# Kernel tuning notes

Hardware: AMD Instinct MI355X
Metric: run time of the kernel (lower is better)

Reference implementation:

```python
import jax, jax.numpy as jnp
import numpy as np

S, D_IN, D_OUT = 4096, 1024, 1024

def setup_inputs() -> dict:
    key = jax.random.key(0)
    kx, kq, kk, kv = jax.random.split(key, 4)
    scale = 0.02
    return {
        "x": jax.random.normal(kx, (S, D_IN), dtype=jnp.float32),
        "W_query": jax.random.normal(kq, (D_IN, D_OUT), dtype=jnp.float32) * scale,
        "W_key": jax.random.normal(kk, (D_IN, D_OUT), dtype=jnp.float32) * scale,
        "W_value": jax.random.normal(kv, (D_IN, D_OUT), dtype=jnp.float32) * scale,
    }

def reference(x, W_query, W_key, W_value):
    # x: [S, d_in]; W_*: [d_in, d_out]
    queries = x @ W_query        # [S, d_out]
    keys = x @ W_key             # [S, d_out]
    values = x @ W_value         # [S, d_out]
    d_k = keys.shape[-1]
    attn_scores = queries @ keys.T            # [S, S]
    attn_weights = jax.nn.softmax(attn_scores / jnp.sqrt(jnp.float32(d_k)), axis=-1)
    context_vec = attn_weights @ values       # [S, d_out]
    return context_vec
```

## Files before the change

### kernel.cpp

```cpp
#include <hip/hip_runtime.h>

typedef _Float16 f16x8 __attribute__((ext_vector_type(8)));
typedef float f32x4 __attribute__((ext_vector_type(4)));
typedef unsigned short u16;
typedef u16 u16x8 __attribute__((ext_vector_type(8)));
typedef u16 u16x4 __attribute__((ext_vector_type(4)));

__device__ __forceinline__ u16 f2h_bits(float f) {
    _Float16 h = (_Float16)f;
    return __builtin_bit_cast(u16, h);
}
__device__ __forceinline__ float h2f(u16 b) {
    return (float)__builtin_bit_cast(_Float16, b);
}

typedef __attribute__((address_space(1))) unsigned int gu32_as1;
typedef __attribute__((address_space(3))) unsigned int lu32_as3;
__device__ __forceinline__ void gload16(const u16* g, u16* l) {
    __builtin_amdgcn_global_load_lds((gu32_as1*)g, (lu32_as3*)l, 16, 0, 0);
}

template <int MODE>
__global__ __launch_bounds__(512, 2) void gemm_bt(
    const u16* __restrict__ A, int lda,
    const u16* __restrict__ B, int ldb,
    u16* __restrict__ C, int ldc,
    int Ksplit, float alpha, size_t c_z_stride,
    int bnW, int bmW, int numPanelX,
    float* __restrict__ rowsum, u16* __restrict__ vt)
{
    __shared__ __attribute__((aligned(16))) u16 As[32768];
    __shared__ __attribute__((aligned(16))) u16 Bs[32768];

    const int t    = threadIdx.x;
    const int lane = t & 63;
    const int wave = t >> 6;
    const int wm   = wave >> 2;
    const int wn   = wave & 3;
    const int l16  = lane & 15;
    const int quad = lane >> 4;

    const int lin = blockIdx.y * gridDim.x + blockIdx.x;
    const int xcd = lin & 7;
    const int idx = lin >> 3;
    const int px  = xcd % numPanelX;
    const int py  = xcd / numPanelX;
    const int bn  = px * bnW + idx % bnW;
    const int bm  = py * bmW + idx / bnW;

    const int kz = blockIdx.z;
    A += (size_t)kz * Ksplit;
    B += (size_t)kz * Ksplit;
    C += (size_t)kz * c_z_stride;

    const int srow = t >> 2;
    const int sseg = (t & 3) ^ ((t >> 3) & 3);

    const u16* gA = A + (size_t)(bm * 256 + srow) * lda + sseg * 8;
    const u16* gB = B + (size_t)(bn * 256 + srow) * ldb + sseg * 8;
    const size_t a128 = (size_t)128 * lda;
    const size_t b128 = (size_t)128 * ldb;

    u16* lA = As + t * 8;
    u16* lB = Bs + t * 8;

#define STAGE_A(bufv, kt) do {                                   \
        const u16* _g = gA + (size_t)(kt) * 64;                  \
        u16* _l = lA + (bufv) * 16384;                           \
        gload16(_g,             _l);                             \
        gload16(_g + 32,        _l + 4096);                      \
        gload16(_g + a128,      _l + 8192);                      \
        gload16(_g + a128 + 32, _l + 12288);                     \
    } while (0)
#define STAGE_B(bufv, kt) do {                                   \
        const u16* _g = gB + (size_t)(kt) * 64;                  \
        u16* _l = lB + (bufv) * 16384;                           \
        gload16(_g,             _l);                             \
        gload16(_g + 32,        _l + 4096);                      \
        gload16(_g + b128,      _l + 8192);                      \
        gload16(_g + b128 + 32, _l + 12288);                     \
    } while (0)

    const int fslot = quad ^ ((l16 >> 1) & 3);
    const u16* Afr = As + wm * 8192 + l16 * 32 + fslot * 8;
    const u16* Bfr = Bs + (wn >> 1) * 8192 + (wn & 1) * 2048 + l16 * 32 + fslot * 8;

    f32x4 acc[8][4] = {};

    const int NT = Ksplit >> 6;

    STAGE_A(0, 0); STAGE_B(0, 0);
    STAGE_A(1, 1); STAGE_B(1, 1);
    asm volatile("s_waitcnt vmcnt(8)" ::: "memory");
    __builtin_amdgcn_sched_barrier(0);
    __builtin_amdgcn_s_barrier();

    int buf = 0;
    for (int kt = 0; kt < NT; ++kt, buf ^= 1) {
        const u16* Af = Afr + buf * 16384;
        const u16* Bf = Bfr + buf * 16384;
        f16x8 af[4][2], bfA[2][2], bfB[2][2];

#pragma unroll
        for (int mi = 0; mi < 4; mi++)
#pragma unroll
            for (int kk = 0; kk < 2; kk++)
                af[mi][kk] = *(const f16x8*)(Af + kk * 4096 + mi * 512);
#pragma unroll
        for (int nj = 0; nj < 2; nj++)
#pragma unroll
            for (int kk = 0; kk < 2; kk++)
                bfA[nj][kk] = *(const f16x8*)(Bf + kk * 4096 + nj * 512);
        __builtin_amdgcn_sched_barrier(0);
        __builtin_amdgcn_s_barrier();
        __builtin_amdgcn_s_setprio(1);
#pragma unroll
        for (int mi = 0; mi < 4; mi++)
#pragma unroll
            for (int nj = 0; nj < 2; nj++)
#pragma unroll
                for (int kk = 0; kk < 2; kk++)
                    acc[mi][nj] = __builtin_amdgcn_mfma_f32_16x16x32_f16(
                        af[mi][kk], bfA[nj][kk], acc[mi][nj], 0, 0, 0);
        __builtin_amdgcn_s_setprio(0);
        __builtin_amdgcn_sched_barrier(0);
        __builtin_amdgcn_s_barrier();

#pragma unroll
        for (int nj = 0; nj < 2; nj++)
#pragma unroll
            for (int kk = 0; kk < 2; kk++)
                bfB[nj][kk] = *(const f16x8*)(Bf + kk * 4096 + (2 + nj) * 512);
        __builtin_amdgcn_sched_barrier(0);
        __builtin_amdgcn_s_barrier();
        __builtin_amdgcn_s_setprio(1);
#pragma unroll
        for (int mi = 0; mi < 4; mi++)
#pragma unroll
            for (int nj = 0; nj < 2; nj++)
#pragma unroll
                for (int kk = 0; kk < 2; kk++)
                    acc[mi][2 + nj] = __builtin_amdgcn_mfma_f32_16x16x32_f16(
                        af[mi][kk], bfB[nj][kk], acc[mi][2 + nj], 0, 0, 0);
        __builtin_amdgcn_s_setprio(0);
        __builtin_amdgcn_sched_barrier(0);
        __builtin_amdgcn_s_barrier();

#pragma unroll
        for (int mi = 0; mi < 4; mi++)
#pragma unroll
            for (int kk = 0; kk < 2; kk++)
                af[mi][kk] = *(const f16x8*)(Af + kk * 4096 + (4 + mi) * 512);
        if (kt + 2 < NT) STAGE_B(buf, kt + 2);
        __builtin_amdgcn_sched_barrier(0);
        __builtin_amdgcn_s_barrier();
        __builtin_amdgcn_s_setprio(1);
#pragma unroll
        for (int mi = 0; mi < 4; mi++)
#pragma unroll
            for (int nj = 0; nj < 2; nj++)
#pragma unroll
                for (int kk = 0; kk < 2; kk++)
                    acc[4 + mi][nj] = __builtin_amdgcn_mfma_f32_16x16x32_f16(
                        af[mi][kk], bfA[nj][kk], acc[4 + mi][nj], 0, 0, 0);
        __builtin_amdgcn_s_setprio(0);
        __builtin_amdgcn_sched_barrier(0);
        __builtin_amdgcn_s_barrier();

        if (kt + 2 < NT) STAGE_A(buf, kt + 2);
        __builtin_amdgcn_sched_barrier(0);
        __builtin_amdgcn_s_barrier();
        __builtin_amdgcn_s_setprio(1);
#pragma unroll
        for (int mi = 0; mi < 4; mi++)
#pragma unroll
            for (int nj = 0; nj < 2; nj++)
#pragma unroll
                for (int kk = 0; kk < 2; kk++)
                    acc[4 + mi][2 + nj] = __builtin_amdgcn_mfma_f32_16x16x32_f16(
                        af[mi][kk], bfB[nj][kk], acc[4 + mi][2 + nj], 0, 0, 0);
        __builtin_amdgcn_s_setprio(0);
        if (kt < NT - 2)       asm volatile("s_waitcnt vmcnt(8)" ::: "memory");
        else if (kt == NT - 2) asm volatile("s_waitcnt vmcnt(0)" ::: "memory");
        __builtin_amdgcn_sched_barrier(0);
        __builtin_amdgcn_s_barrier();
    }
#undef STAGE_A
#undef STAGE_B

    const int crow = bm * 256 + wm * 128 + quad * 4;
    const int ccol = bn * 256 + wn * 64 + l16;

    if (MODE == 1) {
        float rs[8][4];
#pragma unroll
        for (int mi = 0; mi < 8; mi++)
#pragma unroll
            for (int r = 0; r < 4; r++) rs[mi][r] = 0.f;
#pragma unroll
        for (int mi = 0; mi < 8; mi++) {
#pragma unroll
            for (int ni = 0; ni < 4; ni++) {
#pragma unroll
                for (int r = 0; r < 4; r++) {
                    float e = __expf(acc[mi][ni][r] * alpha);
                    rs[mi][r] += e;
                    C[(size_t)(crow + mi * 16 + r) * ldc + (ccol + ni * 16)] = f2h_bits(e);
                }
            }
        }
#pragma unroll
        for (int mi = 0; mi < 8; mi++) {
#pragma unroll
            for (int r = 0; r < 4; r++) {
                float s = rs[mi][r];
#pragma unroll
                for (int o = 1; o < 16; o <<= 1) s += __shfl_xor(s, o);
                if (l16 == 0)
                    atomicAdd(&rowsum[crow + mi * 16 + r], s);
            }
        }
    } else if (MODE == 2 && bn >= 8) {
#pragma unroll
        for (int ni = 0; ni < 4; ni++) {
            const int cV = (bn - 8) * 256 + wn * 64 + ni * 16 + l16;
#pragma unroll
            for (int mi = 0; mi < 8; mi++) {
                u16x4 o;
#pragma unroll
                for (int r = 0; r < 4; r++) o[r] = f2h_bits(acc[mi][ni][r]);
                *(u16x4*)(vt + (size_t)cV * 4096 + crow + mi * 16) = o;
            }
        }
    } else {
#pragma unroll
        for (int mi = 0; mi < 8; mi++)
#pragma unroll
            for (int ni = 0; ni < 4; ni++)
#pragma unroll
                for (int r = 0; r < 4; r++)
                    C[(size_t)(crow + mi * 16 + r) * ldc + (ccol + ni * 16)] =
                        f2h_bits(acc[mi][ni][r] * alpha);
    }
}

__global__ __launch_bounds__(256) void cast_to_f16(
    const float* __restrict__ in, u16* __restrict__ out, int n)
{
    int i = (blockIdx.x * 256 + threadIdx.x) * 4;
    if (i + 3 < n) {
        float4 v = *(const float4*)(in + i);
        ushort4 o;
        o.x = f2h_bits(v.x);
        o.y = f2h_bits(v.y);
        o.z = f2h_bits(v.z);
        o.w = f2h_bits(v.w);
        *(ushort4*)(out + i) = o;
    }
}

__global__ __launch_bounds__(256) void transpose_w3(
    const float* __restrict__ W0, const float* __restrict__ W1,
    const float* __restrict__ W2, u16* __restrict__ out)
{
    const float* in = (blockIdx.z == 0) ? W0 : (blockIdx.z == 1) ? W1 : W2;
    u16* o = out + (size_t)blockIdx.z * 1024 * 1024;
    __shared__ float tile[32][33];
    const int bx = blockIdx.x * 32;
    const int by = blockIdx.y * 32;
    const int tx = threadIdx.x, ty = threadIdx.y;
#pragma unroll
    for (int j = 0; j < 4; j++)
        tile[ty + j * 8][tx] = in[(size_t)(by + ty + j * 8) * 1024 + bx + tx];
    __syncthreads();
#pragma unroll
    for (int j = 0; j < 4; j++)
        o[(size_t)(bx + ty + j * 8) * 1024 + by + tx] = f2h_bits(tile[tx][ty + j * 8]);
}

__global__ __launch_bounds__(256) void zero_f32(float* __restrict__ p, int n)
{
    int i = (blockIdx.x * 256 + threadIdx.x) * 4;
    if (i + 3 < n) *(float4*)(p + i) = float4{0.f, 0.f, 0.f, 0.f};
}

__global__ __launch_bounds__(256) void add_div4(
    const u16* __restrict__ P, const float* __restrict__ l,
    float* __restrict__ o)
{
    const size_t zs = (size_t)4096 * 1024;
    int i = (blockIdx.x * 256 + threadIdx.x) * 8;
    float inv = 1.0f / l[i >> 10];
    float s[8] = {};
#pragma unroll
    for (int z = 0; z < 4; z++) {
        u16x8 h = *(const u16x8*)(P + z * zs + i);
#pragma unroll
        for (int j = 0; j < 8; j++) s[j] += h2f(h[j]);
    }
    float4 lo{s[0] * inv, s[1] * inv, s[2] * inv, s[3] * inv};
    float4 hi{s[4] * inv, s[5] * inv, s[6] * inv, s[7] * inv};
    *(float4*)(o + i) = lo;
    *(float4*)(o + i + 4) = hi;
}

extern "C" void kernel_launch(void* const* d_in, const int* in_sizes, int n_in,
                              void* d_out, int out_size, void* d_ws, size_t ws_size,
                              hipStream_t stream)
{
    (void)in_sizes; (void)n_in; (void)out_size; (void)ws_size;
    const float* x  = (const float*)d_in[0];
    const float* Wq = (const float*)d_in[1];
    const float* Wk = (const float*)d_in[2];
    const float* Wv = (const float*)d_in[3];
    float* out = (float*)d_out;
    char* ws = (char*)d_ws;

    u16* xb  = (u16*)(ws);
    u16* Wt  = (u16*)(ws + ((size_t)8  << 20));
    u16* QK  = (u16*)(ws + ((size_t)14 << 20));
    u16* Sb  = (u16*)(ws + ((size_t)32 << 20));
    u16* Vt  = (u16*)(ws + ((size_t)64 << 20));
    float* lr = (float*)(ws + ((size_t)72 << 20));
    u16* P   = (u16*)(ws);

    const int S = 4096, D = 1024;
    dim3 tb(32, 8);

    cast_to_f16<<<(S * D) / (4 * 256), 256, 0, stream>>>(x, xb, S * D);

    transpose_w3<<<dim3(32, 32, 3), tb, 0, stream>>>(Wq, Wk, Wv, Wt);

    gemm_bt<2><<<dim3(12, 16, 1), 512, 0, stream>>>(
        xb, D, Wt, D, QK, 2048, D, 1.0f, 0, 3, 8, 4, nullptr, Vt);

    zero_f32<<<S / (4 * 256), 256, 0, stream>>>(lr, S);

    gemm_bt<1><<<dim3(16, 16, 1), 512, 0, stream>>>(
        QK, 2048, QK + 1024, 2048, Sb, S, D, 0.03125f, 0, 4, 8, 4, lr, nullptr);

    gemm_bt<0><<<dim3(4, 16, 4), 512, 0, stream>>>(
        Sb, S, Vt, S, P, D, 1024, 1.0f, (size_t)S * D, 1, 8, 4, nullptr, nullptr);

    add_div4<<<(S * D) / (8 * 256), 256, 0, stream>>>(P, lr, out);
}
```

Measured before the change: 219.6 us.

## Collapse eight-phase GEMM main loop into two barrier phases

The K-loop is restructured so each iteration loads all A and B fragments for the tile from LDS up front, then issues the first half of the MFMAs. It then waits for LDS reads, takes a single barrier, issues the A and B global-to-LDS prefetches together, and runs the second half of the MFMAs. This removes most of the per-iteration workgroup barriers and the fine ping-pong interleaving. The cost is higher register pressure, since af0 and af1 are held at once, plus less overlap of LDS reads with MFMA work, which could cause spills at 2 waves/SIMD.

```diff
diff --git a/kernel.cpp b/kernel.cpp
--- a/kernel.cpp
+++ b/kernel.cpp
@@ -94,66 +94,61 @@
     asm volatile("s_waitcnt vmcnt(8)" ::: "memory");
     __builtin_amdgcn_sched_barrier(0);
     __builtin_amdgcn_s_barrier();
-
-    int buf = 0;
-    for (int kt = 0; kt < NT; ++kt, buf ^= 1) {
+    __builtin_amdgcn_sched_barrier(0);
+
+    for (int kt = 0; kt < NT; ++kt) {
+        const int buf = kt & 1;
         const u16* Af = Afr + buf * 16384;
         const u16* Bf = Bfr + buf * 16384;
-        f16x8 af[4][2], bfA[2][2], bfB[2][2];
-
-#pragma unroll
-        for (int mi = 0; mi < 4; mi++)
-#pragma unroll
-            for (int kk = 0; kk < 2; kk++)
-                af[mi][kk] = *(const f16x8*)(Af + kk * 4096 + mi * 512);
+
+        f16x8 bfA[2][2], bfB[2][2], af0[4][2], af1[4][2];
 #pragma unroll
         for (int nj = 0; nj < 2; nj++)
 #pragma unroll
             for (int kk = 0; kk < 2; kk++)
                 bfA[nj][kk] = *(const f16x8*)(Bf + kk * 4096 + nj * 512);
+#pragma unroll
+        for (int mi = 0; mi < 4; mi++)
+#pragma unroll
+            for (int kk = 0; kk < 2; kk++)
+                af0[mi][kk] = *(const f16x8*)(Af + kk * 4096 + mi * 512);
+#pragma unroll
+        for (int nj = 0; nj < 2; nj++)
+#pragma unroll
+            for (int kk = 0; kk < 2; kk++)
+                bfB[nj][kk] = *(const f16x8*)(Bf + kk * 4096 + (2 + nj) * 512);
+#pragma unroll
+        for (int mi = 0; mi < 4; mi++)
+#pragma unroll
+            for (int kk = 0; kk < 2; kk++)
+                af1[mi][kk] = *(const f16x8*)(Af + kk * 4096 + (4 + mi) * 512);
+
+        __builtin_amdgcn_s_setprio(1);
+#pragma unroll
+        for (int mi = 0; mi < 4; mi++)
+#pragma unroll
+            for (int nj = 0; nj < 2; nj++)
+#pragma unroll
+                for (int kk = 0; kk < 2; kk++)
+                    acc[mi][nj] = __builtin_amdgcn_mfma_f32_16x16x32_f16(
+                        af0[mi][kk], bfA[nj][kk], acc[mi][nj], 0, 0, 0);
+#pragma unroll
+        for (int mi = 0; mi < 4; mi++)
+#pragma unroll
+            for (int nj = 0; nj < 2; nj++)
+#pragma unroll
+                for (int kk = 0; kk < 2; kk++)
+                    acc[mi][2 + nj] = __builtin_amdgcn_mfma_f32_16x16x32_f16(
+                        af0[mi][kk], bfB[nj][kk], acc[mi][2 + nj], 0, 0, 0);
+        __builtin_amdgcn_s_setprio(0);
+
+        asm volatile("s_waitcnt lgkmcnt(0)" ::: "memory");
         __builtin_amdgcn_sched_barrier(0);
         __builtin_amdgcn_s_barrier();
-        __builtin_amdgcn_s_setprio(1);
-#pragma unroll
-        for (int mi = 0; mi < 4; mi++)
-#pragma unroll
-            for (int nj = 0; nj < 2; nj++)
-#pragma unroll
-                for (int kk = 0; kk < 2; kk++)
-                    acc[mi][nj] = __builtin_amdgcn_mfma_f32_16x16x32_f16(
-                        af[mi][kk], bfA[nj][kk], acc[mi][nj], 0, 0, 0);
-        __builtin_amdgcn_s_setprio(0);
         __builtin_amdgcn_sched_barrier(0);
-        __builtin_amdgcn_s_barrier();
-
-#pragma unroll
-        for (int nj = 0; nj < 2; nj++)
-#pragma unroll
-            for (int kk = 0; kk < 2; kk++)
-                bfB[nj][kk] = *(const f16x8*)(Bf + kk * 4096 + (2 + nj) * 512);
-        __builtin_amdgcn_sched_barrier(0);
-        __builtin_amdgcn_s_barrier();
-        __builtin_amdgcn_s_setprio(1);
-#pragma unroll
-        for (int mi = 0; mi < 4; mi++)
-#pragma unroll
-            for (int nj = 0; nj < 2; nj++)
-#pragma unroll
-                for (int kk = 0; kk < 2; kk++)
-                    acc[mi][2 + nj] = __builtin_amdgcn_mfma_f32_16x16x32_f16(
-                        af[mi][kk], bfB[nj][kk], acc[mi][2 + nj], 0, 0, 0);
-        __builtin_amdgcn_s_setprio(0);
-        __builtin_amdgcn_sched_barrier(0);
-        __builtin_amdgcn_s_barrier();
-
-#pragma unroll
-        for (int mi = 0; mi < 4; mi++)
-#pragma unroll
-            for (int kk = 0; kk < 2; kk++)
-                af[mi][kk] = *(const f16x8*)(Af + kk * 4096 + (4 + mi) * 512);
-        if (kt + 2 < NT) STAGE_B(buf, kt + 2);
-        __builtin_amdgcn_sched_barrier(0);
-        __builtin_amdgcn_s_barrier();
+
+        if (kt + 2 < NT) { STAGE_A(buf, kt + 2); STAGE_B(buf, kt + 2); }
+
         __builtin_amdgcn_s_setprio(1);
 #pragma unroll
         for (int mi = 0; mi < 4; mi++)
@@ -162,15 +157,7 @@
 #pragma unroll
                 for (int kk = 0; kk < 2; kk++)
                     acc[4 + mi][nj] = __builtin_amdgcn_mfma_f32_16x16x32_f16(
-                        af[mi][kk], bfA[nj][kk], acc[4 + mi][nj], 0, 0, 0);
-        __builtin_amdgcn_s_setprio(0);
-        __builtin_amdgcn_sched_barrier(0);
-        __builtin_amdgcn_s_barrier();
-
-        if (kt + 2 < NT) STAGE_A(buf, kt + 2);
-        __builtin_amdgcn_sched_barrier(0);
-        __builtin_amdgcn_s_barrier();
-        __builtin_amdgcn_s_setprio(1);
+                        af1[mi][kk], bfA[nj][kk], acc[4 + mi][nj], 0, 0, 0);
 #pragma unroll
         for (int mi = 0; mi < 4; mi++)
 #pragma unroll
@@ -178,12 +165,14 @@
 #pragma unroll
                 for (int kk = 0; kk < 2; kk++)
                     acc[4 + mi][2 + nj] = __builtin_amdgcn_mfma_f32_16x16x32_f16(
-                        af[mi][kk], bfB[nj][kk], acc[4 + mi][2 + nj], 0, 0, 0);
+                        af1[mi][kk], bfB[nj][kk], acc[4 + mi][2 + nj], 0, 0, 0);
         __builtin_amdgcn_s_setprio(0);
+
         if (kt < NT - 2)       asm volatile("s_waitcnt vmcnt(8)" ::: "memory");
         else if (kt == NT - 2) asm volatile("s_waitcnt vmcnt(0)" ::: "memory");
         __builtin_amdgcn_sched_barrier(0);
         __builtin_amdgcn_s_barrier();
+        __builtin_amdgcn_sched_barrier(0);
     }
 #undef STAGE_A
 #undef STAGE_B
```

Measured after the change: 214.3 us. -2.4%, faster.
